# Optimization experiments

Measured on AMD Instinct MI355X. Metric: run time of the kernel, lower is better.

The kernel has to match this reference:

```python
import jax, jax.numpy as jnp
import numpy as np

D = 1024
H = 16

def setup_inputs() -> dict:
    key = jax.random.key(0)
    ks = jax.random.split(key, 5)
    x = jax.random.normal(ks[0], (4, 2048, D), dtype=jnp.float32)
    lim = 1.0 / np.sqrt(D)
    W_qkv = jax.random.uniform(ks[1], (D, 3 * D), minval=-lim, maxval=lim, dtype=jnp.float32)
    b_qkv = jax.random.uniform(ks[2], (3 * D,), minval=-lim, maxval=lim, dtype=jnp.float32)
    W_proj = jax.random.uniform(ks[3], (D, D), minval=-lim, maxval=lim, dtype=jnp.float32)
    b_proj = jax.random.uniform(ks[4], (D,), minval=-lim, maxval=lim, dtype=jnp.float32)
    return {"x": x, "W_qkv": W_qkv, "b_qkv": b_qkv, "W_proj": W_proj, "b_proj": b_proj}

def reference(x, W_qkv, b_qkv, W_proj, b_proj):
    B, T, d = x.shape
    hd = d // H
    scale = hd ** (-0.5)
    qkv = x @ W_qkv + b_qkv                       # [B,T,3D]
    qkv = qkv.reshape(B, T, 3, H, hd)
    q = qkv[:, :, 0].transpose(0, 2, 1, 3)        # [B,H,T,hd]
    k = qkv[:, :, 1].transpose(0, 2, 1, 3)
    v = qkv[:, :, 2].transpose(0, 2, 1, 3)
    scores = jnp.einsum('bhqd,bhkd->bhqk', q, k) * scale
    attn = jax.nn.softmax(scores, axis=-1)
    y = jnp.einsum('bhqk,bhkd->bhqd', attn, v)    # [B,H,T,hd]
    y = y.transpose(0, 2, 1, 3).reshape(B, T, d)
    return y @ W_proj + b_proj
```

## Files before the change

kernel.cpp:

```cpp
#include <hip/hip_runtime.h>


typedef __attribute__((ext_vector_type(8))) short bf16x8;
typedef __attribute__((ext_vector_type(8))) unsigned short u16x8;
typedef __attribute__((ext_vector_type(4))) float f32x4;
typedef __attribute__((ext_vector_type(16))) float f32x16;

#define DEV static __device__ __forceinline__

DEV unsigned short f2b(float f) {
  union { float f; unsigned int i; } v; v.f = f;
  unsigned int x = v.i;
  return (unsigned short)((x + 0x7FFFu + ((x >> 16) & 1u)) >> 16);
}

DEV f32x4 mfma16(bf16x8 a, bf16x8 b, f32x4 c) {
  return __builtin_amdgcn_mfma_f32_16x16x32_bf16(a, b, c, 0, 0, 0);
}
DEV f32x16 mfma32(bf16x8 a, bf16x8 b, f32x16 c) {
  return __builtin_amdgcn_mfma_f32_32x32x16_bf16(a, b, c, 0, 0, 0);
}

DEV void gl_lds16(const unsigned short* g, unsigned short* l) {
  __builtin_amdgcn_global_load_lds(
      (const __attribute__((address_space(1))) unsigned int*)g,
      (__attribute__((address_space(3))) unsigned int*)l, 16, 0, 0);
}

DEV void pk_swap(float a0, float a1, float b0, float b1,
                 unsigned int& w_lo, unsigned int& w_hi) {
  unsigned int a, b;
  asm("v_cvt_pk_bf16_f32 %0, %1, %2" : "=v"(a) : "v"(a0), "v"(a1));
  asm("v_cvt_pk_bf16_f32 %0, %1, %2" : "=v"(b) : "v"(b0), "v"(b1));
  asm("v_permlane32_swap_b32 %0, %1" : "+v"(a), "+v"(b));
  w_lo = a; w_hi = b;
}

__global__ __launch_bounds__(256) void f32_to_bf16(
    const float* __restrict__ in, unsigned short* __restrict__ out, int n4) {
  const int i = (blockIdx.x * 256 + threadIdx.x) * 4;
  if (i >= n4 * 4) return;
  const float4 v = *(const float4*)(in + i);
  ushort4 o;
  o.x = f2b(v.x); o.y = f2b(v.y); o.z = f2b(v.z); o.w = f2b(v.w);
  *(ushort4*)(out + i) = o;
}

__global__ __launch_bounds__(256) void transpose_f32_bf16(
    const float* __restrict__ in, unsigned short* __restrict__ out,
    int R, int C) {
  __shared__ float tile[32][33];
  const int tx = threadIdx.x & 31, ty = threadIdx.x >> 5;
  const int c0 = blockIdx.x * 32, r0 = blockIdx.y * 32;
#pragma unroll
  for (int i = 0; i < 32; i += 8)
    tile[ty + i][tx] = in[(size_t)(r0 + ty + i) * C + (c0 + tx)];
  __syncthreads();
#pragma unroll
  for (int i = 0; i < 32; i += 8)
    out[(size_t)(c0 + ty + i) * R + (r0 + tx)] = f2b(tile[tx][ty + i]);
}

__global__ __launch_bounds__(256) void vtrans(
    const unsigned short* __restrict__ in, unsigned short* __restrict__ out) {
  __shared__ __align__(16) unsigned short tile[64 * 72];
  const int tid = threadIdx.x;
  const int bh = blockIdx.y, t0 = blockIdx.x * 64;
  const unsigned short* src = in + (size_t)bh * 131072 + (size_t)t0 * 64;
  unsigned short* dst = out + (size_t)bh * 131072 + t0;
#pragma unroll
  for (int i = 0; i < 2; ++i) {
    const int c = tid + i * 256;
    u16x8 v = *(const u16x8*)(src + c * 8);
    *(u16x8*)&tile[(c >> 3) * 72 + (c & 7) * 8] = v;
  }
  __syncthreads();
#pragma unroll
  for (int i = 0; i < 2; ++i) {
    const int c = tid + i * 256;
    const int d = c >> 3, t8 = (c & 7) * 8;
    u16x8 o;
#pragma unroll
    for (int j = 0; j < 8; ++j) o[j] = tile[(t8 + j) * 72 + d];
    *(u16x8*)(dst + (size_t)d * 2048 + t8) = o;
  }
}

#define QSCALE 0.18033688f
template <int MODE>
__global__ __launch_bounds__(256, 2) void gemm_bt(
    const unsigned short* __restrict__ A, const unsigned short* __restrict__ Bt,
    const float* __restrict__ bias, void* __restrict__ out_v,
    int M, int N, int K) {
  __shared__ __align__(16) unsigned short As[128 * 32];
  __shared__ __align__(16) unsigned short Bs[128 * 32];
  const int tid = threadIdx.x;
  const int w = tid >> 6, l = tid & 63, g = l >> 4, ln = l & 15;
  const int m0 = blockIdx.y * 128, n0 = blockIdx.x * 128;
  const int wm = (w & 1) * 64, wn = (w >> 1) * 64;

  f32x4 acc[4][4];
#pragma unroll
  for (int i = 0; i < 4; ++i)
#pragma unroll
    for (int j = 0; j < 4; ++j) acc[i][j] = (f32x4){0.f, 0.f, 0.f, 0.f};

  const unsigned short* Ab = A + (size_t)m0 * K;
  const unsigned short* Bb = Bt + (size_t)n0 * K;
  const int c0 = tid, c1 = tid + 256;
  const int ar0 = c0 >> 2, ak0 = (c0 & 3) * 8;
  const int ar1 = c1 >> 2, ak1 = (c1 & 3) * 8;

  for (int k0 = 0; k0 < K; k0 += 32) {
    gl_lds16(Ab + (size_t)ar0 * K + k0 + ak0, &As[c0 * 8]);
    gl_lds16(Ab + (size_t)ar1 * K + k0 + ak1, &As[c1 * 8]);
    gl_lds16(Bb + (size_t)ar0 * K + k0 + ak0, &Bs[c0 * 8]);
    gl_lds16(Bb + (size_t)ar1 * K + k0 + ak1, &Bs[c1 * 8]);
    __syncthreads();
    bf16x8 af[4], bf[4];
#pragma unroll
    for (int mi = 0; mi < 4; ++mi)
      af[mi] = *(const bf16x8*)&As[(wm + mi * 16 + ln) * 32 + g * 8];
#pragma unroll
    for (int ni = 0; ni < 4; ++ni)
      bf[ni] = *(const bf16x8*)&Bs[(wn + ni * 16 + ln) * 32 + g * 8];
#pragma unroll
    for (int mi = 0; mi < 4; ++mi)
#pragma unroll
      for (int ni = 0; ni < 4; ++ni)
        acc[mi][ni] = mfma16(af[mi], bf[ni], acc[mi][ni]);
    __syncthreads();
  }

#pragma unroll
  for (int mi = 0; mi < 4; ++mi) {
#pragma unroll
    for (int ni = 0; ni < 4; ++ni) {
      const int row0 = m0 + wm + mi * 16 + 4 * g;
      const int col = n0 + wn + ni * 16 + ln;
      const float bv = bias[col];
#pragma unroll
      for (int r = 0; r < 4; ++r) {
        float v = acc[mi][ni][r] + bv;
        const int row = row0 + r;
        if (MODE == 0) {
          const int which = col >> 10;
          const int h = (col >> 6) & 15;
          const int dd = col & 63;
          const int b = row >> 11, t = row & 2047;
          unsigned short* dst = (unsigned short*)out_v + (size_t)which * 8388608u;
          if (which == 0) v *= QSCALE;
          dst[(((size_t)(b * 16 + h)) * 2048 + t) * 64 + dd] = f2b(v);
        } else {
          ((float*)out_v)[(size_t)row * N + col] = v;
        }
      }
    }
  }
}

__global__ __launch_bounds__(256, 2) void attn(
    const unsigned short* __restrict__ Q, const unsigned short* __restrict__ K,
    const unsigned short* __restrict__ Vtg, unsigned short* __restrict__ Y) {
  __shared__ __align__(16) unsigned short Qs[128 * 72];
  __shared__ __align__(16) unsigned short Ks[64 * 72];
  __shared__ __align__(16) unsigned short Vt[64 * 72];

  const int tid = threadIdx.x;
  const int w = tid >> 6, l = tid & 63;
  const int l32 = l & 31, lh = l >> 5;
  const int bh = blockIdx.y;
  const int q0 = blockIdx.x * 128;

  const unsigned short* Qb = Q + (size_t)bh * 131072;
  const unsigned short* Kb = K + (size_t)bh * 131072;
  const unsigned short* Vb = Vtg + (size_t)bh * 131072;

#pragma unroll
  for (int i = 0; i < 4; ++i) {
    const int c = tid + i * 256;
    u16x8 v = *(const u16x8*)(Qb + (size_t)q0 * 64 + c * 8);
    *(u16x8*)&Qs[(c >> 3) * 72 + (c & 7) * 8] = v;
  }
  __syncthreads();
  bf16x8 aq[4];
#pragma unroll
  for (int kb = 0; kb < 4; ++kb)
    aq[kb] = *(const bf16x8*)&Qs[(w * 32 + l32) * 72 + kb * 16 + lh * 8];

  const short one_b = (short)0x3F80;
  const bf16x8 vones = (bf16x8){one_b, one_b, one_b, one_b,
                                one_b, one_b, one_b, one_b};

  f32x16 o[2], os;
#pragma unroll
  for (int db = 0; db < 2; ++db)
#pragma unroll
    for (int r = 0; r < 16; ++r) o[db][r] = 0.f;
#pragma unroll
  for (int r = 0; r < 16; ++r) os[r] = 0.f;

  for (int kt = 0; kt < 32; ++kt) {
#pragma unroll
    for (int i = 0; i < 2; ++i) {
      const int c = tid + i * 256;
      const int row = c >> 3, cc = (c & 7) * 8;
      u16x8 kv = *(const u16x8*)(Kb + (size_t)kt * 4096 + c * 8);
      u16x8 vv = *(const u16x8*)(Vb + (size_t)row * 2048 + kt * 64 + cc);
      *(u16x8*)&Ks[row * 72 + cc] = kv;
      *(u16x8*)&Vt[row * 72 + cc] = vv;
    }
    __syncthreads();

    f32x16 s[2];
#pragma unroll
    for (int nb = 0; nb < 2; ++nb) {
#pragma unroll
      for (int r = 0; r < 16; ++r) s[nb][r] = 0.f;
#pragma unroll
      for (int kb = 0; kb < 4; ++kb) {
        bf16x8 bk = *(const bf16x8*)&Ks[(nb * 32 + l32) * 72 + kb * 16 + lh * 8];
        s[nb] = mfma32(bk, aq[kb], s[nb]);
      }
    }

    bf16x8 ap[4];
#pragma unroll
    for (int nb = 0; nb < 2; ++nb) {
      float pe[16];
#pragma unroll
      for (int r = 0; r < 16; ++r)
        pe[r] = __builtin_amdgcn_exp2f(s[nb][r]);
      union { unsigned int wd[4]; bf16x8 v; } u0, u1;
      pk_swap(pe[0], pe[1], pe[4], pe[5], u0.wd[0], u0.wd[2]);
      pk_swap(pe[2], pe[3], pe[6], pe[7], u0.wd[1], u0.wd[3]);
      pk_swap(pe[8], pe[9], pe[12], pe[13], u1.wd[0], u1.wd[2]);
      pk_swap(pe[10], pe[11], pe[14], pe[15], u1.wd[1], u1.wd[3]);
      ap[2 * nb + 0] = u0.v;
      ap[2 * nb + 1] = u1.v;
    }

#pragma unroll
    for (int ks = 0; ks < 4; ++ks) {
      os = mfma32(ap[ks], vones, os);
#pragma unroll
      for (int db = 0; db < 2; ++db) {
        bf16x8 bv = *(const bf16x8*)&Vt[(db * 32 + l32) * 72 + ks * 16 + lh * 8];
        o[db] = mfma32(ap[ks], bv, o[db]);
      }
    }
    __syncthreads();
  }

  float iv[16];
#pragma unroll
  for (int r = 0; r < 16; ++r) iv[r] = 1.f / os[r];

  const int b = bh >> 4, h = bh & 15;
#pragma unroll
  for (int db = 0; db < 2; ++db)
#pragma unroll
    for (int r = 0; r < 16; ++r) {
      const int row = (r & 3) + 8 * (r >> 2) + 4 * lh;
      const int t = q0 + w * 32 + row;
      Y[(size_t)(b * 2048 + t) * 1024 + h * 64 + db * 32 + l32] =
          f2b(o[db][r] * iv[r]);
    }
}

extern "C" void kernel_launch(void* const* d_in, const int* in_sizes, int n_in,
                              void* d_out, int out_size, void* d_ws, size_t ws_size,
                              hipStream_t stream) {
  const float* x     = (const float*)d_in[0];
  const float* Wqkv  = (const float*)d_in[1];
  const float* bqkv  = (const float*)d_in[2];
  const float* Wproj = (const float*)d_in[3];
  const float* bproj = (const float*)d_in[4];
  float* out = (float*)d_out;
  unsigned short* ws = (unsigned short*)d_ws;

  unsigned short* xbf    = ws;
  unsigned short* Yw     = xbf;
  unsigned short* WqkvT  = xbf + 8388608;
  unsigned short* WprojT = WqkvT + 3072 * 1024;
  unsigned short* Qw     = WprojT + 1024 * 1024;
  unsigned short* Kw     = Qw + 8388608;
  unsigned short* Vw     = Kw + 8388608;
  unsigned short* Vtw    = Vw + 8388608;

  f32_to_bf16<<<8192, 256, 0, stream>>>(x, xbf, 2097152);
  transpose_f32_bf16<<<dim3(96, 32), 256, 0, stream>>>(Wqkv, WqkvT, 1024, 3072);
  transpose_f32_bf16<<<dim3(32, 32), 256, 0, stream>>>(Wproj, WprojT, 1024, 1024);
  gemm_bt<0><<<dim3(24, 64), 256, 0, stream>>>(xbf, WqkvT, bqkv, Qw, 8192, 3072, 1024);
  vtrans<<<dim3(32, 64), 256, 0, stream>>>(Vw, Vtw);
  attn<<<dim3(16, 64), 256, 0, stream>>>(Qw, Kw, Vtw, Yw);
  gemm_bt<1><<<dim3(8, 64), 256, 0, stream>>>(Yw, WprojT, bproj, out, 8192, 1024, 1024);
}
```

Before: 291.5 us.

## Replace QKV GEMM with 256x256 double-buffered, swizzled, XCD-remapped kernel

Adds a dedicated QKV projection GEMM that uses 256x256 tiles with 512 threads, double-buffered LDS filled by direct global-to-LDS loads, an XOR swizzle against bank conflicts, and an interleaved schedule of fragment reads, prefetch and MFMA phases with explicit waitcnt, barriers and priority hints. Workgroup IDs are remapped across the 8 XCDs to improve L2 locality. It aims to raise MFMA utilisation and hide load latency for the largest GEMM. Larger tiles use 128KB of LDS per block, which can lower occupancy and leave a partial wave of blocks, and the manual waitcnt counts must match the exact load order to stay correct.

New measurement: 300.1 us. +3.0%, slower.

```diff
diff --git a/kernel.cpp b/kernel.cpp
--- a/kernel.cpp
+++ b/kernel.cpp
@@ -7,6 +7,8 @@
 typedef __attribute__((ext_vector_type(16))) float f32x16;
 
 #define DEV static __device__ __forceinline__
+#define SBAR __builtin_amdgcn_sched_barrier(0)
+#define WBAR __builtin_amdgcn_s_barrier()
 
 DEV unsigned short f2b(float f) {
   union { float f; unsigned int i; } v; v.f = f;
@@ -87,10 +89,180 @@
 }
 
 #define QSCALE 0.18033688f
-template <int MODE>
+
+#define STAGE(dst, src, kcol, li)                                        \
+  do {                                                                   \
+    const int ch_ = (li) * 512 + tid;                                    \
+    const int r_ = ch_ >> 3, s_ = ch_ & 7;                               \
+    const int cs_ = (s_ ^ (((r_ >> 2) & 1) << 1)) << 3;                  \
+    gl_lds16((src) + (size_t)r_ * K + (kcol) + cs_, &(dst)[ch_ * 8]);    \
+  } while (0)
+
+DEV bf16x8 rdfrag(const unsigned short* base, int r, int ks, int g) {
+  const int c = (ks * 32 + g * 8) ^ (((r >> 2) & 1) << 4);
+  return *(const bf16x8*)&base[r * 64 + c];
+}
+
+__global__ __launch_bounds__(512, 2) void gemm256_qkv(
+    const unsigned short* __restrict__ A, const unsigned short* __restrict__ Bt,
+    const float* __restrict__ bias, unsigned short* __restrict__ out,
+    int M, int N, int K) {
+  __shared__ __align__(16) unsigned short As[2][16384];
+  __shared__ __align__(16) unsigned short Bs[2][16384];
+  const int tid = threadIdx.x;
+  const int w = tid >> 6, l = tid & 63, g = l >> 4, ln = l & 15;
+  const int wm = (w >> 2) * 128, wn = (w & 3) * 64;
+
+  const int nwgx = gridDim.x;
+  int wg = blockIdx.y * nwgx + blockIdx.x;
+  const int cpx = (nwgx * gridDim.y) >> 3;
+  wg = (wg & 7) * cpx + (wg >> 3);
+  const int m0 = (wg / nwgx) * 256, n0 = (wg % nwgx) * 256;
+
+  const unsigned short* Ab = A + (size_t)m0 * K;
+  const unsigned short* Bb = Bt + (size_t)n0 * K;
+
+  f32x4 acc[8][4];
+#pragma unroll
+  for (int i = 0; i < 8; ++i)
+#pragma unroll
+    for (int j = 0; j < 4; ++j) acc[i][j] = (f32x4){0.f, 0.f, 0.f, 0.f};
+
+  STAGE(Bs[0], Bb, 0, 0); STAGE(Bs[0], Bb, 0, 1);
+  STAGE(Bs[0], Bb, 0, 2); STAGE(Bs[0], Bb, 0, 3);
+  STAGE(As[0], Ab, 0, 0); STAGE(As[0], Ab, 0, 2);
+  STAGE(As[0], Ab, 0, 1); STAGE(As[0], Ab, 0, 3);
+  asm volatile("s_waitcnt vmcnt(0)" ::: "memory");
+  WBAR;
+
+  const int NT = K >> 6;
+  for (int T = 0; T < NT; ++T) {
+    unsigned short* Acur = (unsigned short*)As[T & 1];
+    unsigned short* Bcur = (unsigned short*)Bs[T & 1];
+    unsigned short* Anxt = (unsigned short*)As[(T & 1) ^ 1];
+    unsigned short* Bnxt = (unsigned short*)Bs[(T & 1) ^ 1];
+    const bool hn = (T + 1) < NT;
+    const int kn = (T + 1) * 64;
+
+    bf16x8 bfr[4][2];
+    {
+      bf16x8 aq[2][2];
+#pragma unroll
+      for (int mi = 0; mi < 2; ++mi)
+#pragma unroll
+        for (int ks = 0; ks < 2; ++ks)
+          aq[mi][ks] = rdfrag(Acur, wm + (0 + mi) * 16 + ln, ks, g);
+#pragma unroll
+      for (int ni = 0; ni < 4; ++ni)
+#pragma unroll
+        for (int ks = 0; ks < 2; ++ks)
+          bfr[ni][ks] = rdfrag(Bcur, wn + ni * 16 + ln, ks, g);
+      if (hn) { STAGE(Bnxt, Bb, kn, 0); STAGE(Bnxt, Bb, kn, 1); }
+      SBAR; WBAR; SBAR;
+      __builtin_amdgcn_s_setprio(1);
+#pragma unroll
+      for (int ks = 0; ks < 2; ++ks)
+#pragma unroll
+        for (int mi = 0; mi < 2; ++mi)
+#pragma unroll
+          for (int ni = 0; ni < 4; ++ni)
+            acc[0 + mi][ni] = mfma16(aq[mi][ks], bfr[ni][ks], acc[0 + mi][ni]);
+      __builtin_amdgcn_s_setprio(0);
+      SBAR; WBAR;
+    }
+    {
+      bf16x8 aq[2][2];
+#pragma unroll
+      for (int mi = 0; mi < 2; ++mi)
+#pragma unroll
+        for (int ks = 0; ks < 2; ++ks)
+          aq[mi][ks] = rdfrag(Acur, wm + (2 + mi) * 16 + ln, ks, g);
+      if (hn) { STAGE(Bnxt, Bb, kn, 2); STAGE(Bnxt, Bb, kn, 3); }
+      SBAR; WBAR; SBAR;
+      __builtin_amdgcn_s_setprio(1);
+#pragma unroll
+      for (int ks = 0; ks < 2; ++ks)
+#pragma unroll
+        for (int mi = 0; mi < 2; ++mi)
+#pragma unroll
+          for (int ni = 0; ni < 4; ++ni)
+            acc[2 + mi][ni] = mfma16(aq[mi][ks], bfr[ni][ks], acc[2 + mi][ni]);
+      __builtin_amdgcn_s_setprio(0);
+      SBAR;
+      if (hn) asm volatile("s_waitcnt vmcnt(4)" ::: "memory");
+      else    asm volatile("s_waitcnt vmcnt(0)" ::: "memory");
+      SBAR; WBAR;
+    }
+    {
+      bf16x8 aq[2][2];
+#pragma unroll
+      for (int mi = 0; mi < 2; ++mi)
+#pragma unroll
+        for (int ks = 0; ks < 2; ++ks)
+          aq[mi][ks] = rdfrag(Acur, wm + (4 + mi) * 16 + ln, ks, g);
+      if (hn) { STAGE(Anxt, Ab, kn, 0); STAGE(Anxt, Ab, kn, 2); }
+      SBAR; WBAR; SBAR;
+      __builtin_amdgcn_s_setprio(1);
+#pragma unroll
+      for (int ks = 0; ks < 2; ++ks)
+#pragma unroll
+        for (int mi = 0; mi < 2; ++mi)
+#pragma unroll
+          for (int ni = 0; ni < 4; ++ni)
+            acc[4 + mi][ni] = mfma16(aq[mi][ks], bfr[ni][ks], acc[4 + mi][ni]);
+      __builtin_amdgcn_s_setprio(0);
+      SBAR; WBAR;
+    }
+    {
+      bf16x8 aq[2][2];
+#pragma unroll
+      for (int mi = 0; mi < 2; ++mi)
+#pragma unroll
+        for (int ks = 0; ks < 2; ++ks)
+          aq[mi][ks] = rdfrag(Acur, wm + (6 + mi) * 16 + ln, ks, g);
+      if (hn) { STAGE(Anxt, Ab, kn, 1); STAGE(Anxt, Ab, kn, 3); }
+      SBAR; WBAR; SBAR;
+      __builtin_amdgcn_s_setprio(1);
+#pragma unroll
+      for (int ks = 0; ks < 2; ++ks)
+#pragma unroll
+        for (int mi = 0; mi < 2; ++mi)
+#pragma unroll
+          for (int ni = 0; ni < 4; ++ni)
+            acc[6 + mi][ni] = mfma16(aq[mi][ks], bfr[ni][ks], acc[6 + mi][ni]);
+      __builtin_amdgcn_s_setprio(0);
+      SBAR;
+      if (hn) asm volatile("s_waitcnt vmcnt(2)" ::: "memory");
+      SBAR; WBAR;
+    }
+  }
+
+#pragma unroll
+  for (int mi = 0; mi < 8; ++mi) {
+#pragma unroll
+    for (int ni = 0; ni < 4; ++ni) {
+      const int row0 = m0 + wm + mi * 16 + 4 * g;
+      const int col = n0 + wn + ni * 16 + ln;
+      const float bv = bias[col];
+      const int which = col >> 10;
+      const int h = (col >> 6) & 15;
+      const int dd = col & 63;
+      unsigned short* dst = out + (size_t)which * 8388608u;
+#pragma unroll
+      for (int r = 0; r < 4; ++r) {
+        float v = acc[mi][ni][r] + bv;
+        const int row = row0 + r;
+        const int b = row >> 11, t = row & 2047;
+        if (which == 0) v *= QSCALE;
+        dst[(((size_t)(b * 16 + h)) * 2048 + t) * 64 + dd] = f2b(v);
+      }
+    }
+  }
+}
+
 __global__ __launch_bounds__(256, 2) void gemm_bt(
     const unsigned short* __restrict__ A, const unsigned short* __restrict__ Bt,
-    const float* __restrict__ bias, void* __restrict__ out_v,
+    const float* __restrict__ bias, float* __restrict__ out,
     int M, int N, int K) {
   __shared__ __align__(16) unsigned short As[128 * 32];
   __shared__ __align__(16) unsigned short Bs[128 * 32];
@@ -140,21 +312,8 @@
       const int col = n0 + wn + ni * 16 + ln;
       const float bv = bias[col];
 #pragma unroll
-      for (int r = 0; r < 4; ++r) {
-        float v = acc[mi][ni][r] + bv;
-        const int row = row0 + r;
-        if (MODE == 0) {
-          const int which = col >> 10;
-          const int h = (col >> 6) & 15;
-          const int dd = col & 63;
-          const int b = row >> 11, t = row & 2047;
-          unsigned short* dst = (unsigned short*)out_v + (size_t)which * 8388608u;
-          if (which == 0) v *= QSCALE;
-          dst[(((size_t)(b * 16 + h)) * 2048 + t) * 64 + dd] = f2b(v);
-        } else {
-          ((float*)out_v)[(size_t)row * N + col] = v;
-        }
-      }
+      for (int r = 0; r < 4; ++r)
+        out[(size_t)(row0 + r) * N + col] = acc[mi][ni][r] + bv;
     }
   }
 }
@@ -291,8 +450,8 @@
   f32_to_bf16<<<8192, 256, 0, stream>>>(x, xbf, 2097152);
   transpose_f32_bf16<<<dim3(96, 32), 256, 0, stream>>>(Wqkv, WqkvT, 1024, 3072);
   transpose_f32_bf16<<<dim3(32, 32), 256, 0, stream>>>(Wproj, WprojT, 1024, 1024);
-  gemm_bt<0><<<dim3(24, 64), 256, 0, stream>>>(xbf, WqkvT, bqkv, Qw, 8192, 3072, 1024);
+  gemm256_qkv<<<dim3(12, 32), 512, 0, stream>>>(xbf, WqkvT, bqkv, Qw, 8192, 3072, 1024);
   vtrans<<<dim3(32, 64), 256, 0, stream>>>(Vw, Vtw);
   attn<<<dim3(16, 64), 256, 0, stream>>>(Qw, Kw, Vtw, Yw);
-  gemm_bt<1><<<dim3(8, 64), 256, 0, stream>>>(Yw, WprojT, bproj, out, 8192, 1024, 1024);
-}
+  gemm_bt<<<dim3(8, 64), 256, 0, stream>>>(Yw, WprojT, bproj, out, 8192, 1024, 1024);
+}
```

## Double-buffer K/V tiles in attention kernel with register prefetch

Applied to the files above, without the earlier changes.

The attention kernel now keeps two LDS buffers for K and V. The next tile's global loads are issued into registers before the current tile's MFMA work and written to the alternate buffer afterwards. This overlaps global memory latency with compute and removes one barrier per iteration. In exchange it doubles K/V LDS usage and adds 16 live registers per thread, which could affect occupancy at 2 blocks per CU.

Result: faster. 279.3 us (-4.2%).

```diff
diff --git a/kernel.cpp b/kernel.cpp
--- a/kernel.cpp
+++ b/kernel.cpp
@@ -163,8 +163,8 @@
     const unsigned short* __restrict__ Q, const unsigned short* __restrict__ K,
     const unsigned short* __restrict__ Vtg, unsigned short* __restrict__ Y) {
   __shared__ __align__(16) unsigned short Qs[128 * 72];
-  __shared__ __align__(16) unsigned short Ks[64 * 72];
-  __shared__ __align__(16) unsigned short Vt[64 * 72];
+  __shared__ __align__(16) unsigned short Ks[2][64 * 72];
+  __shared__ __align__(16) unsigned short Vt[2][64 * 72];
 
   const int tid = threadIdx.x;
   const int w = tid >> 6, l = tid & 63;
@@ -176,13 +176,26 @@
   const unsigned short* Kb = K + (size_t)bh * 131072;
   const unsigned short* Vb = Vtg + (size_t)bh * 131072;
 
+  const int c0 = tid, c1 = tid + 256;
+  const int r0 = c0 >> 3, s0 = (c0 & 7) * 8;
+  const int r1 = c1 >> 3, s1 = (c1 & 7) * 8;
+
+  u16x8 ka = *(const u16x8*)(Kb + c0 * 8);
+  u16x8 kb2 = *(const u16x8*)(Kb + c1 * 8);
+  u16x8 va = *(const u16x8*)(Vb + (size_t)r0 * 2048 + s0);
+  u16x8 vb2 = *(const u16x8*)(Vb + (size_t)r1 * 2048 + s1);
 #pragma unroll
   for (int i = 0; i < 4; ++i) {
     const int c = tid + i * 256;
-    u16x8 v = *(const u16x8*)(Qb + (size_t)q0 * 64 + c * 8);
-    *(u16x8*)&Qs[(c >> 3) * 72 + (c & 7) * 8] = v;
-  }
+    u16x8 qv = *(const u16x8*)(Qb + (size_t)q0 * 64 + c * 8);
+    *(u16x8*)&Qs[(c >> 3) * 72 + (c & 7) * 8] = qv;
+  }
+  *(u16x8*)&Ks[0][r0 * 72 + s0] = ka;
+  *(u16x8*)&Ks[0][r1 * 72 + s1] = kb2;
+  *(u16x8*)&Vt[0][r0 * 72 + s0] = va;
+  *(u16x8*)&Vt[0][r1 * 72 + s1] = vb2;
   __syncthreads();
+
   bf16x8 aq[4];
 #pragma unroll
   for (int kb = 0; kb < 4; ++kb)
@@ -201,16 +214,22 @@
   for (int r = 0; r < 16; ++r) os[r] = 0.f;
 
   for (int kt = 0; kt < 32; ++kt) {
-#pragma unroll
-    for (int i = 0; i < 2; ++i) {
-      const int c = tid + i * 256;
-      const int row = c >> 3, cc = (c & 7) * 8;
-      u16x8 kv = *(const u16x8*)(Kb + (size_t)kt * 4096 + c * 8);
-      u16x8 vv = *(const u16x8*)(Vb + (size_t)row * 2048 + kt * 64 + cc);
-      *(u16x8*)&Ks[row * 72 + cc] = kv;
-      *(u16x8*)&Vt[row * 72 + cc] = vv;
-    }
-    __syncthreads();
+    const int cur = kt & 1;
+    const unsigned short* Kc = Ks[cur];
+    const unsigned short* Vc = Vt[cur];
+    unsigned short* Kn = (unsigned short*)Ks[cur ^ 1];
+    unsigned short* Vn = (unsigned short*)Vt[cur ^ 1];
+    const bool more = (kt + 1) < 32;
+
+    u16x8 kn0, kn1, vn0, vn1;
+    if (more) {
+      const size_t kof = (size_t)(kt + 1) * 4096;
+      const int vof = (kt + 1) * 64;
+      kn0 = *(const u16x8*)(Kb + kof + c0 * 8);
+      kn1 = *(const u16x8*)(Kb + kof + c1 * 8);
+      vn0 = *(const u16x8*)(Vb + (size_t)r0 * 2048 + vof + s0);
+      vn1 = *(const u16x8*)(Vb + (size_t)r1 * 2048 + vof + s1);
+    }
 
     f32x16 s[2];
 #pragma unroll
@@ -219,7 +238,7 @@
       for (int r = 0; r < 16; ++r) s[nb][r] = 0.f;
 #pragma unroll
       for (int kb = 0; kb < 4; ++kb) {
-        bf16x8 bk = *(const bf16x8*)&Ks[(nb * 32 + l32) * 72 + kb * 16 + lh * 8];
+        bf16x8 bk = *(const bf16x8*)&Kc[(nb * 32 + l32) * 72 + kb * 16 + lh * 8];
         s[nb] = mfma32(bk, aq[kb], s[nb]);
       }
     }
@@ -245,9 +264,16 @@
       os = mfma32(ap[ks], vones, os);
 #pragma unroll
       for (int db = 0; db < 2; ++db) {
-        bf16x8 bv = *(const bf16x8*)&Vt[(db * 32 + l32) * 72 + ks * 16 + lh * 8];
+        bf16x8 bv = *(const bf16x8*)&Vc[(db * 32 + l32) * 72 + ks * 16 + lh * 8];
         o[db] = mfma32(ap[ks], bv, o[db]);
       }
+    }
+
+    if (more) {
+      *(u16x8*)&Kn[r0 * 72 + s0] = kn0;
+      *(u16x8*)&Kn[r1 * 72 + s1] = kn1;
+      *(u16x8*)&Vn[r0 * 72 + s0] = vn0;
+      *(u16x8*)&Vn[r1 * 72 + s1] = vn1;
     }
     __syncthreads();
   }
```
